# Optimization experiments

Hardware: AMD Instinct MI355X
Metric: run time of the kernel (lower is better)

Reference implementation:

```python
import jax, jax.numpy as jnp
import numpy as np

B, IN_UNITS, C, J, D = 256, 8, 1152, 10, 16  # batch, capsule-in dim, in_channels, num_units, unit_size
N_ITERS = 4


def squash(s, axis):
    # Faithful to the torch version: s += 1e-5 happens BEFORE computing magnitudes.
    s = s + 1e-5
    mag_sq = jnp.sum(s * s, axis=axis, keepdims=True)
    return mag_sq / (1.0 + mag_sq) * (s / jnp.sqrt(mag_sq))


def setup_inputs() -> dict:
    key = jax.random.key(0)
    k1, k2 = jax.random.split(key)
    x = jax.random.normal(k1, (B, IN_UNITS, C), dtype=jnp.float32)
    W = jax.random.normal(k2, (1, C, J, D, IN_UNITS), dtype=jnp.float32)
    return {"x": x, "W": W}


def reference(x, W):
    # x: (B, in_units, in_channels) -> transpose to (B, C, K) with K = in_units
    xt = jnp.transpose(x, (0, 2, 1))
    # u_hat[b,c,j,d] = sum_k W[0,c,j,d,k] * xt[b,c,k]   (B, C, J, D)
    u_hat = jnp.einsum('cjdk,bck->bcjd', W[0], xt)
    # b_ij is shared across the batch in the original: shape (1, C, J, 1)
    b_ij = jnp.zeros((C, J), dtype=u_hat.dtype)
    v_j = None
    for _ in range(N_ITERS):
        c_ij = jax.nn.softmax(b_ij, axis=1)                 # softmax over num_units J
        s_j = jnp.einsum('cj,bcjd->bjd', c_ij, u_hat)       # sum over input capsules C
        v_j = squash(s_j, axis=-1)                          # squash over unit_size D
        # agreement summed over unit_size AND batch (matches sum(dim=0) in torch)
        agreement = jnp.einsum('bcjd,bjd->cj', u_hat, v_j)
        b_ij = b_ij + agreement
    # torch returns v_j.squeeze(1) with shape (B, J, D, 1)
    return v_j[..., None]
```

## Files before the change

kernel.cpp:

```cpp
#include <hip/hip_runtime.h>
#include <hip/hip_fp16.h>


typedef float v2f __attribute__((ext_vector_type(2)));

#define C_IN  1152
#define J_U   10
#define M_DIM 9216
#define N_DIM 160
#define B_SZ  256

#define OFF_XT 0
#define OFF_U  2400000
#define OFF_SP 26000000
#define OFF_B0 26400000
#define OFF_B1 26420000
#define OFF_AG 26440000

__global__ __launch_bounds__(256) void k_prep(const float* __restrict__ x,
                                              float* __restrict__ Xt) {
    __shared__ float T[64][65];
    const int bid = blockIdx.x, t = threadIdx.x;
    const int m0 = (bid % 144) * 64, b0 = (bid / 144) * 64;
    {
        const int b_l = t >> 2, q = t & 3;
        const float* xp = x + (size_t)(b0 + b_l) * M_DIM + m0 + q * 16;
#pragma unroll
        for (int u = 0; u < 4; ++u) {
            const float4 v = *reinterpret_cast<const float4*>(xp + 4 * u);
            T[q * 16 + 4 * u + 0][b_l] = v.x;
            T[q * 16 + 4 * u + 1][b_l] = v.y;
            T[q * 16 + 4 * u + 2][b_l] = v.z;
            T[q * 16 + 4 * u + 3][b_l] = v.w;
        }
    }
    __syncthreads();
    {
        const int m_l = t >> 2, q = t & 3;
        float4* op = reinterpret_cast<float4*>(Xt + (size_t)(m0 + m_l) * B_SZ + b0 + q * 16);
#pragma unroll
        for (int u = 0; u < 4; ++u)
            op[u] = make_float4(T[m_l][q * 16 + 4 * u], T[m_l][q * 16 + 4 * u + 1],
                                T[m_l][q * 16 + 4 * u + 2], T[m_l][q * 16 + 4 * u + 3]);
    }
}

__global__ __launch_bounds__(256) void k_ubuild(const float* __restrict__ Xt,
                                                const float* __restrict__ W,
                                                __half2* __restrict__ U2) {
    __shared__ float Wl[2880];
    const int cc = blockIdx.x >> 3, nc = blockIdx.x & 7;
    const int c0 = cc * 18, n0 = nc * 20;
    const int t = threadIdx.x;
    const float4* W4 = reinterpret_cast<const float4*>(W);
    float4* Wl4 = reinterpret_cast<float4*>(Wl);
    for (int i = t; i < 720; i += 256) {
        const int c = i / 40, r = i - c * 40;
        const int n = r >> 1, half = r & 1;
        Wl4[i] = W4[(size_t)(c0 + c) * 320 + (n0 + n) * 2 + half];
    }
    __syncthreads();
    const int b2 = t & 127, ch = t >> 7;
    for (int ci = 0; ci < 9; ++ci) {
        const int c = ch * 9 + ci;
        v2f xk[8];
#pragma unroll
        for (int k = 0; k < 8; ++k)
            xk[k] = *reinterpret_cast<const v2f*>(
                Xt + (size_t)(k * C_IN + c0 + c) * B_SZ + 2 * b2);
#pragma unroll
        for (int n = 0; n < 20; ++n) {
            v2f acc = {0.f, 0.f};
            const float* wp = &Wl[(c * 20 + n) * 8];
#pragma unroll
            for (int k = 0; k < 8; ++k) {
                const float w = wp[k];
                acc += xk[k] * (v2f){w, w};
            }
            U2[((size_t)(n0 + n) * C_IN + c0 + c) * 128 + b2] =
                __floats2half2_rn(acc.x, acc.y);
        }
    }
}

__global__ __launch_bounds__(256) void k_gemvs(const __half2* __restrict__ U2,
                                               const float* __restrict__ bij_old,
                                               float* __restrict__ bij_new,
                                               const float* __restrict__ agg,
                                               float* __restrict__ s_part,
                                               int first) {
    __shared__ float braw[1440];
    __shared__ float csm[144];
    const int ce = blockIdx.x / 80, np = blockIdx.x % 80;
    const int c0 = ce * 144, n0 = np * 2, j = np >> 3;
    const int t = threadIdx.x;
    if (first) {
        for (int c = t; c < 144; c += 256) csm[c] = 0.1f;
        if (np == 0)
            for (int i = t; i < 1440; i += 256) bij_new[c0 * J_U + i] = 0.f;
    } else {
        for (int i = t; i < 1440; i += 256) {
            const float v = bij_old[c0 * J_U + i] + agg[c0 * J_U + i];
            braw[i] = v;
            if (np == 0) bij_new[c0 * J_U + i] = v;
        }
        __syncthreads();
        for (int c = t; c < 144; c += 256) {
            const int r0 = c * J_U;
            float mx = -1e30f;
#pragma unroll
            for (int q = 0; q < J_U; ++q) mx = fmaxf(mx, braw[r0 + q]);
            float sum = 0.f;
#pragma unroll
            for (int q = 0; q < J_U; ++q) sum += __expf(braw[r0 + q] - mx);
            csm[c] = __expf(braw[r0 + j] - mx) / sum;
        }
    }
    __syncthreads();
    const int b2 = t & 127, nh = t >> 7;
    const int nn = n0 + nh;
    const __half2* up = U2 + ((size_t)nn * C_IN + c0) * 128 + b2;
    v2f acc = {0.f, 0.f};
#pragma unroll 8
    for (int c = 0; c < 144; ++c) {
        const float2 f = __half22float2(up[(size_t)c * 128]);
        const float cs = csm[c];
        acc += (v2f){cs, cs} * (v2f){f.x, f.y};
    }
    *reinterpret_cast<float2*>(s_part + (size_t)ce * 40960 + (size_t)nn * B_SZ + 2 * b2) =
        make_float2(acc.x, acc.y);
}

__global__ __launch_bounds__(256) void k_agree(const __half2* __restrict__ U2,
                                               const float* __restrict__ s_part,
                                               float* __restrict__ agg) {
    __shared__ float sv[16 * 256];
    __shared__ float red[12 * 128];
    const int j = blockIdx.x / 96, cc = blockIdx.x % 96;
    const int c0 = cc * 12;
    const int t = threadIdx.x;
    for (int i = t; i < 4096; i += 256) {
        const int d = i >> 8, b = i & 255;
        const float* p = s_part + (size_t)(j * 16 + d) * B_SZ + b;
        float s = 1e-5f;
#pragma unroll
        for (int ce = 0; ce < 8; ++ce) s += p[(size_t)ce * 40960];
        sv[d * 256 + b] = s;
    }
    __syncthreads();
    {
        float mag = 0.f;
#pragma unroll
        for (int d = 0; d < 16; ++d) { const float xx = sv[d * 256 + t]; mag += xx * xx; }
        const float sc = sqrtf(mag) / (1.f + mag);
#pragma unroll
        for (int d = 0; d < 16; ++d) sv[d * 256 + t] *= sc;
    }
    __syncthreads();
    const int b2 = t & 127, ch = t >> 7;
    float acc[6] = {};
#pragma unroll
    for (int ci = 0; ci < 6; ++ci) {
        const int c = c0 + ch * 6 + ci;
        const __half2* up = U2 + ((size_t)(j * 16) * C_IN + c) * 128 + b2;
#pragma unroll
        for (int d = 0; d < 16; ++d) {
            const float2 f = __half22float2(up[(size_t)d * C_IN * 128]);
            const float2 vv = *reinterpret_cast<const float2*>(&sv[d * 256 + 2 * b2]);
            acc[ci] += f.x * vv.x + f.y * vv.y;
        }
    }
#pragma unroll
    for (int ci = 0; ci < 6; ++ci) red[(ch * 6 + ci) * 128 + b2] = acc[ci];
    __syncthreads();
#pragma unroll
    for (int pass = 0; pass < 3; ++pass) {
        const int r = pass * 4 + (t >> 6), l = t & 63;
        float v = red[r * 128 + l] + red[r * 128 + l + 64];
#pragma unroll
        for (int off = 32; off > 0; off >>= 1) v += __shfl_down(v, off);
        if (l == 0) agg[(size_t)(c0 + r) * J_U + j] = v;
    }
}

__global__ __launch_bounds__(256) void k_sqout(const float* __restrict__ s_part,
                                               float* __restrict__ out) {
    __shared__ float sl[16 * 32];
    const int j = blockIdx.x >> 3, bc = blockIdx.x & 7;
    const int b0 = bc * 32;
    const int t = threadIdx.x;
    for (int i = t; i < 512; i += 256) {
        const int d = i >> 5, bl = i & 31;
        const float* p = s_part + (size_t)(j * 16 + d) * B_SZ + b0 + bl;
        float s = 1e-5f;
#pragma unroll
        for (int ce = 0; ce < 8; ++ce) s += p[(size_t)ce * 40960];
        sl[d * 32 + bl] = s;
    }
    __syncthreads();
    if (t < 32) {
        float mag = 0.f;
#pragma unroll
        for (int d = 0; d < 16; ++d) { const float xx = sl[d * 32 + t]; mag += xx * xx; }
        const float sc = sqrtf(mag) / (1.f + mag);
#pragma unroll
        for (int d = 0; d < 16; ++d)
            out[(size_t)(b0 + t) * N_DIM + j * 16 + d] = sl[d * 32 + t] * sc;
    }
}

extern "C" void kernel_launch(void* const* d_in, const int* in_sizes, int n_in,
                              void* d_out, int out_size, void* d_ws, size_t ws_size,
                              hipStream_t stream) {
    const float* x = (const float*)d_in[0];
    const float* W = (const float*)d_in[1];
    float* out = (float*)d_out;
    float* ws  = (float*)d_ws;
    float* Xt   = ws + OFF_XT;
    __half2* U2 = (__half2*)(ws + OFF_U);
    float* sp   = ws + OFF_SP;
    float* bij0 = ws + OFF_B0;
    float* bij1 = ws + OFF_B1;
    float* agg  = ws + OFF_AG;

    k_prep<<<576, 256, 0, stream>>>(x, Xt);
    k_ubuild<<<512, 256, 0, stream>>>(Xt, W, U2);

    for (int it = 0; it < 4; ++it) {
        const float* bo = (it & 1) ? bij1 : bij0;
        float*       bn = (it & 1) ? bij0 : bij1;
        k_gemvs<<<640, 256, 0, stream>>>(U2, bo, bn, agg, sp, it == 0 ? 1 : 0);
        if (it < 3)
            k_agree<<<960, 256, 0, stream>>>(U2, sp, agg);
    }
    k_sqout<<<80, 256, 0, stream>>>(sp, out);
}
```

Measured before the change: 216.7 us.

## Fuse first routing iteration's weighted sum into u_hat build kernel

The uniform-coupling first iteration (c=0.1) is folded into k_ubuild: each block accumulates its u_hat values in fp32 and writes per-chunk partial sums (32 slices), removing one full k_gemvs pass over U2. The k_ubuild tiling changes to 36 channels by 10 outputs per block so partials can be produced, and k_agree accepts a variable slice count. Block indices in k_ubuild and k_agree are remapped, likely to spread work across XCDs or improve cache locality. The first partial sums now come from unrounded fp32 rather than the fp16 U2, which slightly changes numerics.

```diff
diff --git a/kernel.cpp b/kernel.cpp
--- a/kernel.cpp
+++ b/kernel.cpp
@@ -10,12 +10,13 @@
 #define N_DIM 160
 #define B_SZ  256
 
-#define OFF_XT 0
-#define OFF_U  2400000
-#define OFF_SP 26000000
-#define OFF_B0 26400000
-#define OFF_B1 26420000
-#define OFF_AG 26440000
+#define OFF_XT  0
+#define OFF_U   2400000
+#define OFF_SP8 26000000
+#define OFF_SP32 26400000
+#define OFF_B0  27800000
+#define OFF_B1  27820000
+#define OFF_AG  27840000
 
 __global__ __launch_bounds__(256) void k_prep(const float* __restrict__ x,
                                               float* __restrict__ Xt) {
@@ -47,31 +48,35 @@
 
 __global__ __launch_bounds__(256) void k_ubuild(const float* __restrict__ Xt,
                                                 const float* __restrict__ W,
-                                                __half2* __restrict__ U2) {
+                                                __half2* __restrict__ U2,
+                                                float* __restrict__ s32) {
     __shared__ float Wl[2880];
-    const int cc = blockIdx.x >> 3, nc = blockIdx.x & 7;
-    const int c0 = cc * 18, n0 = nc * 20;
+    __shared__ v2f Sred[2][10][128];
+    const int vb = (blockIdx.x & 7) * 64 + (blockIdx.x >> 3);
+    const int cc = vb >> 4, nc = vb & 15;
+    const int c0 = cc * 36, n0 = nc * 10;
     const int t = threadIdx.x;
     const float4* W4 = reinterpret_cast<const float4*>(W);
     float4* Wl4 = reinterpret_cast<float4*>(Wl);
     for (int i = t; i < 720; i += 256) {
-        const int c = i / 40, r = i - c * 40;
+        const int c = i / 20, r = i - c * 20;
         const int n = r >> 1, half = r & 1;
         Wl4[i] = W4[(size_t)(c0 + c) * 320 + (n0 + n) * 2 + half];
     }
     __syncthreads();
     const int b2 = t & 127, ch = t >> 7;
-    for (int ci = 0; ci < 9; ++ci) {
-        const int c = ch * 9 + ci;
+    v2f sacc[10] = {};
+    for (int ci = 0; ci < 18; ++ci) {
+        const int c = ch * 18 + ci;
         v2f xk[8];
 #pragma unroll
         for (int k = 0; k < 8; ++k)
             xk[k] = *reinterpret_cast<const v2f*>(
                 Xt + (size_t)(k * C_IN + c0 + c) * B_SZ + 2 * b2);
 #pragma unroll
-        for (int n = 0; n < 20; ++n) {
+        for (int n = 0; n < 10; ++n) {
             v2f acc = {0.f, 0.f};
-            const float* wp = &Wl[(c * 20 + n) * 8];
+            const float* wp = &Wl[(c * 10 + n) * 8];
 #pragma unroll
             for (int k = 0; k < 8; ++k) {
                 const float w = wp[k];
@@ -79,7 +84,18 @@
             }
             U2[((size_t)(n0 + n) * C_IN + c0 + c) * 128 + b2] =
                 __floats2half2_rn(acc.x, acc.y);
+            sacc[n] += acc;
         }
+    }
+#pragma unroll
+    for (int n = 0; n < 10; ++n) Sred[ch][n][b2] = sacc[n];
+    __syncthreads();
+    for (int i = t; i < 1280; i += 256) {
+        const int n = i >> 7, bi = i & 127;
+        const v2f s = Sred[0][n][bi] + Sred[1][n][bi];
+        *reinterpret_cast<float2*>(
+            s32 + ((size_t)cc * N_DIM + n0 + n) * B_SZ + 2 * bi) =
+            make_float2(0.1f * s.x, 0.1f * s.y);
     }
 }
 
@@ -88,33 +104,28 @@
                                                float* __restrict__ bij_new,
                                                const float* __restrict__ agg,
                                                float* __restrict__ s_part,
-                                               int first) {
+                                               int nobij) {
     __shared__ float braw[1440];
     __shared__ float csm[144];
     const int ce = blockIdx.x / 80, np = blockIdx.x % 80;
     const int c0 = ce * 144, n0 = np * 2, j = np >> 3;
     const int t = threadIdx.x;
-    if (first) {
-        for (int c = t; c < 144; c += 256) csm[c] = 0.1f;
-        if (np == 0)
-            for (int i = t; i < 1440; i += 256) bij_new[c0 * J_U + i] = 0.f;
-    } else {
-        for (int i = t; i < 1440; i += 256) {
-            const float v = bij_old[c0 * J_U + i] + agg[c0 * J_U + i];
-            braw[i] = v;
-            if (np == 0) bij_new[c0 * J_U + i] = v;
-        }
-        __syncthreads();
-        for (int c = t; c < 144; c += 256) {
-            const int r0 = c * J_U;
-            float mx = -1e30f;
-#pragma unroll
-            for (int q = 0; q < J_U; ++q) mx = fmaxf(mx, braw[r0 + q]);
-            float sum = 0.f;
-#pragma unroll
-            for (int q = 0; q < J_U; ++q) sum += __expf(braw[r0 + q] - mx);
-            csm[c] = __expf(braw[r0 + j] - mx) / sum;
-        }
+    for (int i = t; i < 1440; i += 256) {
+        float v = agg[c0 * J_U + i];
+        if (!nobij) v += bij_old[c0 * J_U + i];
+        braw[i] = v;
+        if (np == 0) bij_new[c0 * J_U + i] = v;
+    }
+    __syncthreads();
+    for (int c = t; c < 144; c += 256) {
+        const int r0 = c * J_U;
+        float mx = -1e30f;
+#pragma unroll
+        for (int q = 0; q < J_U; ++q) mx = fmaxf(mx, braw[r0 + q]);
+        float sum = 0.f;
+#pragma unroll
+        for (int q = 0; q < J_U; ++q) sum += __expf(braw[r0 + q] - mx);
+        csm[c] = __expf(braw[r0 + j] - mx) / sum;
     }
     __syncthreads();
     const int b2 = t & 127, nh = t >> 7;
@@ -132,19 +143,21 @@
 }
 
 __global__ __launch_bounds__(256) void k_agree(const __half2* __restrict__ U2,
-                                               const float* __restrict__ s_part,
+                                               const float* __restrict__ s_base,
+                                               int nsl,
                                                float* __restrict__ agg) {
     __shared__ float sv[16 * 256];
     __shared__ float red[12 * 128];
-    const int j = blockIdx.x / 96, cc = blockIdx.x % 96;
+    const int vb = (blockIdx.x & 7) * 120 + (blockIdx.x >> 3);
+    const int j = vb / 96, cc = vb % 96;
     const int c0 = cc * 12;
     const int t = threadIdx.x;
     for (int i = t; i < 4096; i += 256) {
         const int d = i >> 8, b = i & 255;
-        const float* p = s_part + (size_t)(j * 16 + d) * B_SZ + b;
+        const float* p = s_base + (size_t)(j * 16 + d) * B_SZ + b;
         float s = 1e-5f;
-#pragma unroll
-        for (int ce = 0; ce < 8; ++ce) s += p[(size_t)ce * 40960];
+#pragma unroll 8
+        for (int ce = 0; ce < nsl; ++ce) s += p[(size_t)ce * 40960];
         sv[d * 256 + b] = s;
     }
     __syncthreads();
@@ -218,20 +231,19 @@
     float* ws  = (float*)d_ws;
     float* Xt   = ws + OFF_XT;
     __half2* U2 = (__half2*)(ws + OFF_U);
-    float* sp   = ws + OFF_SP;
+    float* sp8  = ws + OFF_SP8;
+    float* sp32 = ws + OFF_SP32;
     float* bij0 = ws + OFF_B0;
     float* bij1 = ws + OFF_B1;
     float* agg  = ws + OFF_AG;
 
     k_prep<<<576, 256, 0, stream>>>(x, Xt);
-    k_ubuild<<<512, 256, 0, stream>>>(Xt, W, U2);
-
-    for (int it = 0; it < 4; ++it) {
-        const float* bo = (it & 1) ? bij1 : bij0;
-        float*       bn = (it & 1) ? bij0 : bij1;
-        k_gemvs<<<640, 256, 0, stream>>>(U2, bo, bn, agg, sp, it == 0 ? 1 : 0);
-        if (it < 3)
-            k_agree<<<960, 256, 0, stream>>>(U2, sp, agg);
-    }
-    k_sqout<<<80, 256, 0, stream>>>(sp, out);
-}
+    k_ubuild<<<512, 256, 0, stream>>>(Xt, W, U2, sp32);
+    k_agree<<<960, 256, 0, stream>>>(U2, sp32, 32, agg);
+    k_gemvs<<<640, 256, 0, stream>>>(U2, bij1, bij0, agg, sp8, 1);
+    k_agree<<<960, 256, 0, stream>>>(U2, sp8, 8, agg);
+    k_gemvs<<<640, 256, 0, stream>>>(U2, bij0, bij1, agg, sp8, 0);
+    k_agree<<<960, 256, 0, stream>>>(U2, sp8, 8, agg);
+    k_gemvs<<<640, 256, 0, stream>>>(U2, bij1, bij0, agg, sp8, 0);
+    k_sqout<<<80, 256, 0, stream>>>(sp8, out);
+}
```

Result: slower. 245.5 us (+13.3%).
